# Performance work log

Hardware: AMD Instinct MI355X
Metric: run time of the kernel (lower is better)

## Reference

```python
import jax, jax.numpy as jnp
import numpy as np

N_HEAD = 12
NUM_BLOCK_TOKENS = 64
SSMAX_S_INIT = 0.43


def setup_inputs() -> dict:
    key = jax.random.key(0)
    k1, k2, k3 = jax.random.split(key, 3)
    B, T, C = 2, 2048, 768
    x = jax.random.normal(k1, (B, T, C), dtype=jnp.float32)
    # torch Linear weights: y = x @ W.T ; init scaled for stability
    c_attn_w = jax.random.normal(k2, (3 * C, C), dtype=jnp.float32) * 0.02
    c_proj_w = jax.random.normal(k3, (C, C), dtype=jnp.float32) * 0.02
    s = jnp.full((1,), SSMAX_S_INIT, dtype=jnp.float32)  # learnable SSMax scale
    return {"x": x, "c_attn_w": c_attn_w, "c_proj_w": c_proj_w, "s": s}


def reference(x, c_attn_w, c_proj_w, s):
    B, T, C = x.shape
    H, hd, n = N_HEAD, C // N_HEAD, NUM_BLOCK_TOKENS
    qkv = x @ c_attn_w.T                              # [B,T,3C]
    q, k, v = jnp.split(qkv, 3, axis=-1)
    q = q.reshape(B, T, H, hd).transpose(0, 2, 1, 3)  # [B,H,T,hd]
    k = k.reshape(B, T, H, hd).transpose(0, 2, 1, 3)
    v = v.reshape(B, T, H, hd).transpose(0, 2, 1, 3)
    att = jnp.einsum('bhqd,bhkd->bhqk', q, k) * (1.0 / np.sqrt(hd))
    # slot-based block mask reduces to block-causal: allow s_idx//n <= t_idx//n
    blk = jnp.arange(T) // n
    mask = blk[:, None] >= blk[None, :]               # [T,T] bool, True=attend
    scale = s[0] * np.log(T).astype(np.float32)       # SSMax: s * log(N)
    att = jnp.where(mask[None, None], att * scale, -jnp.inf)
    att = jax.nn.softmax(att, axis=-1)
    y = jnp.einsum('bhqk,bhkd->bhqd', att, v)
    y = y.transpose(0, 2, 1, 3).reshape(B, T, C)
    return y @ c_proj_w.T
```

## Files before the change

### kernel.cpp

```cpp
#include <hip/hip_runtime.h>
#include <hip/hip_bf16.h>
#include <stdint.h>

#define T_SEQ 2048
#define C_DIM 768
#define NH 12
#define HD 64
#define QK_LD 1536

typedef __attribute__((ext_vector_type(8))) short short8;
typedef __attribute__((ext_vector_type(4))) float f32x4;
typedef const __attribute__((address_space(1))) void* gas_ptr;
typedef __attribute__((address_space(3))) void* las_ptr;

static __device__ __forceinline__ unsigned short f2bf(float f) {
  union { float f; unsigned u; } c; c.f = f;
  unsigned u = c.u + 0x7fffu + ((c.u >> 16) & 1u);
  return (unsigned short)(u >> 16);
}

__global__ void cast3_kernel(const float* __restrict__ a, int na4,
                             const float* __restrict__ b, int nb4,
                             const float* __restrict__ c, int nc4,
                             unsigned short* __restrict__ oa,
                             unsigned short* __restrict__ ob,
                             unsigned short* __restrict__ oc) {
  int i = blockIdx.x * blockDim.x + threadIdx.x;
  int stride = gridDim.x * blockDim.x;
  int total = na4 + nb4 + nc4;
  for (; i < total; i += stride) {
    const float4* src; ushort4* dst; int j;
    if (i < na4)            { src = (const float4*)a; dst = (ushort4*)oa; j = i; }
    else if (i < na4 + nb4) { src = (const float4*)b; dst = (ushort4*)ob; j = i - na4; }
    else                    { src = (const float4*)c; dst = (ushort4*)oc; j = i - na4 - nb4; }
    float4 v = src[j];
    ushort4 o;
    o.x = f2bf(v.x); o.y = f2bf(v.y); o.z = f2bf(v.z); o.w = f2bf(v.w);
    dst[j] = o;
  }
}

__global__ void zero2_kernel(float4* __restrict__ a, int n4a,
                             float4* __restrict__ b, int n4b) {
  int i = blockIdx.x * blockDim.x + threadIdx.x;
  int stride = gridDim.x * blockDim.x;
  float4 z = {0.f, 0.f, 0.f, 0.f};
  for (int j = i; j < n4a; j += stride) a[j] = z;
  for (int j = i; j < n4b; j += stride) b[j] = z;
}

template <int NP>
__device__ __forceinline__ void stage_tile(const unsigned short* g, int ld,
                                           unsigned short* ldsbase, int tid) {
#pragma unroll
  for (int p = 0; p < NP; ++p) {
    int j = p * 256 + tid;
    int row = j >> 2, cc = (j & 3) << 3;
    const unsigned short* ga = g + (size_t)row * ld + cc;
    unsigned short* la = ldsbase + p * 2048 + (tid >> 6) * 512;
    __builtin_amdgcn_global_load_lds((gas_ptr)ga, (las_ptr)la, 16, 0, 0);
  }
}

template <int BM, int EPI>
__launch_bounds__(256, 2)
__global__ void gemm_bt(const unsigned short* __restrict__ A,
                        const unsigned short* __restrict__ B,
                        int K,
                        unsigned short* __restrict__ obf,
                        unsigned short* __restrict__ vt,
                        float* __restrict__ ofp,
                        const float* __restrict__ sptr) {
  constexpr int MI = BM / 32;
  constexpr int LDS_SH = BM * 32 + 4096;
  constexpr int TR_SH = (EPI == 0) ? 128 * 130 : 0;
  constexpr int TOT = LDS_SH > TR_SH ? LDS_SH : TR_SH;
  __shared__ __attribute__((aligned(16))) unsigned short smem[TOT];
  unsigned short* lds = smem;
  int tid = threadIdx.x;
  int lane = tid & 63, wave = tid >> 6;
  int row0 = blockIdx.x * BM, col0 = blockIdx.y * 128;
  int wr = (wave >> 1) * (BM / 2), wc = (wave & 1) * 64;
  int la = lane & 15, lb = lane >> 4;
  f32x4 acc[MI][4] = {};

  for (int k0 = 0; k0 < K; k0 += 32) {
    __syncthreads();
    stage_tile<BM / 64>(A + (size_t)row0 * K + k0, K, lds, tid);
    stage_tile<2>(B + (size_t)col0 * K + k0, K, lds + BM * 32, tid);
    __syncthreads();
    short8 af[MI], bfr[4];
#pragma unroll
    for (int i = 0; i < MI; ++i)
      af[i] = *(const short8*)&lds[(wr + i * 16 + la) * 32 + lb * 8];
#pragma unroll
    for (int j = 0; j < 4; ++j)
      bfr[j] = *(const short8*)&lds[BM * 32 + (wc + j * 16 + la) * 32 + lb * 8];
#pragma unroll
    for (int i = 0; i < MI; ++i)
#pragma unroll
      for (int j = 0; j < 4; ++j)
        acc[i][j] = __builtin_amdgcn_mfma_f32_16x16x32_bf16(af[i], bfr[j], acc[i][j], 0, 0, 0);
  }

  if (EPI == 0 && col0 >= 1536) {
    __syncthreads();
#pragma unroll
    for (int i = 0; i < MI; ++i)
#pragma unroll
      for (int j = 0; j < 4; ++j)
#pragma unroll
        for (int r = 0; r < 4; ++r)
          smem[(wr + i * 16 + lb * 4 + r) * 130 + (wc + j * 16 + la)] =
              f2bf(acc[i][j][r]);
    __syncthreads();
    int bb = row0 >> 11, t0 = row0 & 2047;
    int cl = tid >> 1, half = tid & 1;
    int vcol = col0 - 1536 + cl;
    int h = vcol >> 6, d = vcol & 63;
    unsigned short* dst =
        vt + ((size_t)(bb * NH + h) * 64 + d) * T_SEQ + t0 + half * 64;
#pragma unroll
    for (int j = 0; j < 8; ++j) {
      short8 v8;
#pragma unroll
      for (int e = 0; e < 8; ++e)
        v8[e] = (short)smem[(half * 64 + j * 8 + e) * 130 + cl];
      *(short8*)(dst + j * 8) = v8;
    }
    return;
  }

  float qs = 0.f;
  if (EPI == 0)
    qs = sptr[0] * 7.624618986159398f  * 0.125f
         * 1.4426950408889634f ;
#pragma unroll
  for (int i = 0; i < MI; ++i) {
    int gr0 = row0 + wr + i * 16 + lb * 4;
#pragma unroll
    for (int j = 0; j < 4; ++j) {
      int gc = col0 + wc + j * 16 + la;
#pragma unroll
      for (int r = 0; r < 4; ++r) {
        float v = acc[i][j][r];
        int rr = gr0 + r;
        if (EPI == 0) {
          obf[(size_t)rr * QK_LD + gc] = f2bf(gc < 768 ? v * qs : v);
        } else {
          ofp[(size_t)rr * C_DIM + gc] = v;
        }
      }
    }
  }
}

__device__ __forceinline__ void attn_stage(const unsigned short* kg,
                                           const unsigned short* vg,
                                           char* kbuf, int wave, int lane) {
  int l3 = lane >> 3;
  int cg = ((lane & 7) ^ l3) << 4;
#pragma unroll
  for (int q = 0; q < 2; ++q) {
    int rk = q * 32 + wave * 8 + l3;
    const unsigned short* ka = kg + (size_t)rk * QK_LD + (cg >> 1);
    char* kl = kbuf + (q * 32 + wave * 8) * 128;
    __builtin_amdgcn_global_load_lds((gas_ptr)ka, (las_ptr)kl, 16, 0, 0);
    const unsigned short* va = vg + (size_t)rk * T_SEQ + (cg >> 1);
    char* vl = kbuf + 8192 + (q * 32 + wave * 8) * 128;
    __builtin_amdgcn_global_load_lds((gas_ptr)va, (las_ptr)vl, 16, 0, 0);
  }
}

__launch_bounds__(256, 4)
__global__ void attn_kernel(const unsigned short* __restrict__ qkb,
                            const unsigned short* __restrict__ vt,
                            float* __restrict__ yp,
                            float* __restrict__ lsp) {
  __shared__ __attribute__((aligned(16))) char smem[2 * 16384 + 8192];

  int tid = threadIdx.x, lane = tid & 63, wave = tid >> 6;
  int la = lane & 15, lb = lane >> 4;
  int xx = 47 - (int)blockIdx.x;
  int qi, cch;
  if (xx < 16) { qi = xx; cch = 0; }
  else         { int t = xx - 16; qi = 16 + (t >> 1); cch = t & 1; }
  int kt0 = cch * 16;
  int kt1 = min(qi, kt0 + 15);
  int bh = blockIdx.y;
  int b = bh / NH, h = bh - b * NH;

  const unsigned short* qbase =
      qkb + ((size_t)(b * T_SEQ + qi * 64 + wave * 16 + la)) * QK_LD + h * HD;
  short8 qf0 = *(const short8*)(qbase + lb * 8);
  short8 qf1 = *(const short8*)(qbase + 32 + lb * 8);
  asm volatile("" :: "v"(qf0), "v"(qf1));

  f32x4 y[4] = {};
  float ls[4] = {0.f, 0.f, 0.f, 0.f};

  const unsigned short* kg0 = qkb + (size_t)b * T_SEQ * QK_LD + 768 + h * HD;
  const unsigned short* vg0 = vt + (size_t)bh * 64 * T_SEQ;
  char* pw = smem + 32768 + wave * 2048;

  attn_stage(kg0 + (size_t)kt0 * 64 * QK_LD, vg0 + kt0 * 64, smem, wave, lane);
  int cur = 0;

  for (int kt = kt0; kt <= kt1; ++kt) {
    asm volatile("" ::: "memory");
    __builtin_amdgcn_s_barrier();
    if (kt < kt1) {
      attn_stage(kg0 + (size_t)(kt + 1) * 64 * QK_LD, vg0 + (kt + 1) * 64,
                 smem + ((cur ^ 1) * 16384), wave, lane);
      asm volatile("s_waitcnt vmcnt(4)" ::: "memory");
    } else {
      asm volatile("s_waitcnt vmcnt(0)" ::: "memory");
    }
    __builtin_amdgcn_s_barrier();
    asm volatile("" ::: "memory");
    __builtin_amdgcn_sched_barrier(0);

    char* kl = smem + cur * 16384;
    char* vl = kl + 8192;

    f32x4 s[4] = {};
    __builtin_amdgcn_s_setprio(1);
#pragma unroll
    for (int fk = 0; fk < 4; ++fk) {
      int row = fk * 16 + la;
      {
        int off = (row * 128 + 0 * 64 + lb * 16) ^ ((row & 7) << 4);
        short8 kf = *(const short8*)(kl + off);
        s[fk] = __builtin_amdgcn_mfma_f32_16x16x32_bf16(qf0, kf, s[fk], 0, 0, 0);
      }
      {
        int off = (row * 128 + 1 * 64 + lb * 16) ^ ((row & 7) << 4);
        short8 kf = *(const short8*)(kl + off);
        s[fk] = __builtin_amdgcn_mfma_f32_16x16x32_bf16(qf1, kf, s[fk], 0, 0, 0);
      }
    }
    __builtin_amdgcn_s_setprio(0);

#pragma unroll
    for (int fk = 0; fk < 4; ++fk)
#pragma unroll
      for (int r = 0; r < 4; ++r) {
        float p = __builtin_amdgcn_exp2f(s[fk][r]);
        s[fk][r] = p;
        ls[r] += p;
        int row = lb * 4 + r;
        int off = (row * 128 + (fk * 16 + la) * 2) ^ ((row & 7) << 4);
        *(unsigned short*)(pw + off) = f2bf(p);
      }

    short8 pa[2];
#pragma unroll
    for (int ch = 0; ch < 2; ++ch) {
      int off = (la * 128 + ch * 64 + lb * 16) ^ ((la & 7) << 4);
      pa[ch] = *(const short8*)(pw + off);
    }
    __builtin_amdgcn_s_setprio(1);
#pragma unroll
    for (int fd = 0; fd < 4; ++fd) {
      int row = fd * 16 + la;
#pragma unroll
      for (int ch = 0; ch < 2; ++ch) {
        int off = (row * 128 + ch * 64 + lb * 16) ^ ((row & 7) << 4);
        short8 vf = *(const short8*)(vl + off);
        y[fd] = __builtin_amdgcn_mfma_f32_16x16x32_bf16(pa[ch], vf, y[fd], 0, 0, 0);
      }
    }
    __builtin_amdgcn_s_setprio(0);

    cur ^= 1;
  }

  size_t slotbase = (size_t)cch * (24 * 2048);
#pragma unroll
  for (int r = 0; r < 4; ++r) {
    float v = ls[r];
    v += __shfl_xor(v, 1); v += __shfl_xor(v, 2);
    v += __shfl_xor(v, 4); v += __shfl_xor(v, 8);
    ls[r] = v;
  }
  int trow = qi * 64 + wave * 16 + lb * 4;
  if (la == 0) {
#pragma unroll
    for (int r = 0; r < 4; ++r)
      lsp[slotbase + (size_t)bh * 2048 + trow + r] = ls[r];
  }
  float* ydst = yp + (slotbase + (size_t)bh * 2048) * 64;
#pragma unroll
  for (int fd = 0; fd < 4; ++fd)
#pragma unroll
    for (int r = 0; r < 4; ++r)
      ydst[(size_t)(trow + r) * 64 + fd * 16 + la] = y[fd][r];
}

__global__ void norm_kernel(const float* __restrict__ yp,
                            const float* __restrict__ lsp,
                            unsigned short* __restrict__ yb) {
  int gid = blockIdx.x * blockDim.x + threadIdx.x;
  int dq = gid & 15;
  int row = gid >> 4;
  int bh = row >> 11, t = row & 2047;
  int b = bh / NH, h = bh - b * NH;
  float denom = lsp[row] + lsp[24 * 2048 + row];
  float inv = 1.0f / denom;
  float4 y0 = ((const float4*)yp)[row * 16 + dq];
  float4 y1 = ((const float4*)yp)[(24 * 2048 * 16) + row * 16 + dq];
  ushort4 o;
  o.x = f2bf((y0.x + y1.x) * inv);
  o.y = f2bf((y0.y + y1.y) * inv);
  o.z = f2bf((y0.z + y1.z) * inv);
  o.w = f2bf((y0.w + y1.w) * inv);
  ((ushort4*)yb)[(size_t)(b * T_SEQ + t) * 192 + h * 16 + dq] = o;
}

extern "C" void kernel_launch(void* const* d_in, const int* in_sizes, int n_in,
                              void* d_out, int out_size, void* d_ws, size_t ws_size,
                              hipStream_t stream) {
  const float* x = (const float*)d_in[0];
  const float* attn_w = (const float*)d_in[1];
  const float* proj_w = (const float*)d_in[2];
  const float* s = (const float*)d_in[3];
  float* out = (float*)d_out;

  char* ws = (char*)d_ws;
  unsigned short* xb  = (unsigned short*)(ws);
  unsigned short* wab = (unsigned short*)(ws + 6291456);
  unsigned short* wpb = (unsigned short*)(ws + 9830400);
  unsigned short* qkb = (unsigned short*)(ws + 11010048);
  unsigned short* vtb = (unsigned short*)(ws + 23592960);
  unsigned short* yb  = (unsigned short*)(ws + 29884416);
  float*          yp  = (float*)(ws + 36175872);
  float*          lsp = (float*)(ws + 61341696);

  cast3_kernel<<<2048, 256, 0, stream>>>(x, 3145728 / 4, attn_w, 1769472 / 4,
                                         proj_w, 589824 / 4, xb, wab, wpb);

  zero2_kernel<<<1024, 256, 0, stream>>>((float4*)(yp + 24 * 2048 * 64), 786432,
                                         (float4*)(lsp + 24 * 2048), 12288);

  gemm_bt<128, 0><<<dim3(32, 18), 256, 0, stream>>>(xb, wab, 768, qkb, vtb, nullptr, s);

  attn_kernel<<<dim3(48, 24), 256, 0, stream>>>(qkb, vtb, yp, lsp);

  norm_kernel<<<3072, 256, 0, stream>>>(yp, lsp, yb);

  gemm_bt<64, 1><<<dim3(64, 6), 256, 0, stream>>>(yb, wpb, 768, nullptr, nullptr, out, nullptr);
}
```

Measured before the change: 163.7 us.

## Double-buffer GEMM LDS, remap blocks per XCD, normalize single-chunk attention rows in-kernel

The GEMM K loop now double-buffers LDS tiles, prefetching the next K slice while MFMAs run on the current one, and occupancy hints are raised. Block indices in both the GEMMs and the attention kernel are remapped so neighbouring tiles land on the same XCD, aiming at better L2 reuse. Attention blocks for the first 16 query tiles, which have only one key chunk, normalize and write bf16 output directly. This removes the zero kernel and halves the norm kernel's work. The changes cost extra LDS per block and more complex index arithmetic.

```diff
diff --git a/kernel.cpp b/kernel.cpp
--- a/kernel.cpp
+++ b/kernel.cpp
@@ -40,15 +40,6 @@
   }
 }
 
-__global__ void zero2_kernel(float4* __restrict__ a, int n4a,
-                             float4* __restrict__ b, int n4b) {
-  int i = blockIdx.x * blockDim.x + threadIdx.x;
-  int stride = gridDim.x * blockDim.x;
-  float4 z = {0.f, 0.f, 0.f, 0.f};
-  for (int j = i; j < n4a; j += stride) a[j] = z;
-  for (int j = i; j < n4b; j += stride) b[j] = z;
-}
-
 template <int NP>
 __device__ __forceinline__ void stage_tile(const unsigned short* g, int ld,
                                            unsigned short* ldsbase, int tid) {
@@ -62,8 +53,8 @@
   }
 }
 
-template <int BM, int EPI>
-__launch_bounds__(256, 2)
+template <int BM, int EPI, int NY, int PERX>
+__launch_bounds__(256, EPI == 0 ? 3 : 4)
 __global__ void gemm_bt(const unsigned short* __restrict__ A,
                         const unsigned short* __restrict__ B,
                         int K,
@@ -72,39 +63,51 @@
                         float* __restrict__ ofp,
                         const float* __restrict__ sptr) {
   constexpr int MI = BM / 32;
-  constexpr int LDS_SH = BM * 32 + 4096;
+  constexpr int ABUF = BM * 32;
+  constexpr int BUF = ABUF + 4096;
+  constexpr int LDS_SH = 2 * BUF;
   constexpr int TR_SH = (EPI == 0) ? 128 * 130 : 0;
   constexpr int TOT = LDS_SH > TR_SH ? LDS_SH : TR_SH;
   __shared__ __attribute__((aligned(16))) unsigned short smem[TOT];
-  unsigned short* lds = smem;
   int tid = threadIdx.x;
   int lane = tid & 63, wave = tid >> 6;
-  int row0 = blockIdx.x * BM, col0 = blockIdx.y * 128;
+  int L = blockIdx.x;
+  int t0 = (L & 7) * PERX + (L >> 3);
+  int row0 = (t0 / NY) * BM, col0 = (t0 % NY) * 128;
   int wr = (wave >> 1) * (BM / 2), wc = (wave & 1) * 64;
   int la = lane & 15, lb = lane >> 4;
   f32x4 acc[MI][4] = {};
 
-  for (int k0 = 0; k0 < K; k0 += 32) {
-    __syncthreads();
-    stage_tile<BM / 64>(A + (size_t)row0 * K + k0, K, lds, tid);
-    stage_tile<2>(B + (size_t)col0 * K + k0, K, lds + BM * 32, tid);
-    __syncthreads();
+  const unsigned short* Abase = A + (size_t)row0 * K;
+  const unsigned short* Bbase = B + (size_t)col0 * K;
+  stage_tile<BM / 64>(Abase, K, smem, tid);
+  stage_tile<2>(Bbase, K, smem + ABUF, tid);
+  __syncthreads();
+  int cur = 0;
+  int nt = K >> 5;
+  for (int t = 0; t < nt; ++t) {
+    if (t + 1 < nt) {
+      stage_tile<BM / 64>(Abase + (t + 1) * 32, K, smem + (cur ^ 1) * BUF, tid);
+      stage_tile<2>(Bbase + (t + 1) * 32, K, smem + (cur ^ 1) * BUF + ABUF, tid);
+    }
+    unsigned short* lds = smem + cur * BUF;
     short8 af[MI], bfr[4];
 #pragma unroll
     for (int i = 0; i < MI; ++i)
       af[i] = *(const short8*)&lds[(wr + i * 16 + la) * 32 + lb * 8];
 #pragma unroll
     for (int j = 0; j < 4; ++j)
-      bfr[j] = *(const short8*)&lds[BM * 32 + (wc + j * 16 + la) * 32 + lb * 8];
+      bfr[j] = *(const short8*)&lds[ABUF + (wc + j * 16 + la) * 32 + lb * 8];
 #pragma unroll
     for (int i = 0; i < MI; ++i)
 #pragma unroll
       for (int j = 0; j < 4; ++j)
         acc[i][j] = __builtin_amdgcn_mfma_f32_16x16x32_bf16(af[i], bfr[j], acc[i][j], 0, 0, 0);
+    __syncthreads();
+    cur ^= 1;
   }
 
   if (EPI == 0 && col0 >= 1536) {
-    __syncthreads();
 #pragma unroll
     for (int i = 0; i < MI; ++i)
 #pragma unroll
@@ -114,12 +117,12 @@
           smem[(wr + i * 16 + lb * 4 + r) * 130 + (wc + j * 16 + la)] =
               f2bf(acc[i][j][r]);
     __syncthreads();
-    int bb = row0 >> 11, t0 = row0 & 2047;
+    int bb = row0 >> 11, t0r = row0 & 2047;
     int cl = tid >> 1, half = tid & 1;
     int vcol = col0 - 1536 + cl;
     int h = vcol >> 6, d = vcol & 63;
     unsigned short* dst =
-        vt + ((size_t)(bb * NH + h) * 64 + d) * T_SEQ + t0 + half * 64;
+        vt + ((size_t)(bb * NH + h) * 64 + d) * T_SEQ + t0r + half * 64;
 #pragma unroll
     for (int j = 0; j < 8; ++j) {
       short8 v8;
@@ -176,18 +179,21 @@
 __global__ void attn_kernel(const unsigned short* __restrict__ qkb,
                             const unsigned short* __restrict__ vt,
                             float* __restrict__ yp,
-                            float* __restrict__ lsp) {
+                            float* __restrict__ lsp,
+                            unsigned short* __restrict__ yb) {
   __shared__ __attribute__((aligned(16))) char smem[2 * 16384 + 8192];
 
   int tid = threadIdx.x, lane = tid & 63, wave = tid >> 6;
   int la = lane & 15, lb = lane >> 4;
-  int xx = 47 - (int)blockIdx.x;
+  int L = blockIdx.x;
+  int ixcd = L >> 3;
+  int bh = (L & 7) * 3 + ixcd / 48;
+  int xx = 47 - (ixcd % 48);
   int qi, cch;
   if (xx < 16) { qi = xx; cch = 0; }
   else         { int t = xx - 16; qi = 16 + (t >> 1); cch = t & 1; }
   int kt0 = cch * 16;
   int kt1 = min(qi, kt0 + 15);
-  int bh = blockIdx.y;
   int b = bh / NH, h = bh - b * NH;
 
   const unsigned short* qbase =
@@ -275,7 +281,6 @@
     cur ^= 1;
   }
 
-  size_t slotbase = (size_t)cch * (24 * 2048);
 #pragma unroll
   for (int r = 0; r < 4; ++r) {
     float v = ls[r];
@@ -284,17 +289,33 @@
     ls[r] = v;
   }
   int trow = qi * 64 + wave * 16 + lb * 4;
-  if (la == 0) {
-#pragma unroll
-    for (int r = 0; r < 4; ++r)
-      lsp[slotbase + (size_t)bh * 2048 + trow + r] = ls[r];
-  }
-  float* ydst = yp + (slotbase + (size_t)bh * 2048) * 64;
-#pragma unroll
-  for (int fd = 0; fd < 4; ++fd)
-#pragma unroll
-    for (int r = 0; r < 4; ++r)
-      ydst[(size_t)(trow + r) * 64 + fd * 16 + la] = y[fd][r];
+
+  if (qi < 16) {
+    float inv[4];
+#pragma unroll
+    for (int r = 0; r < 4; ++r) inv[r] = 1.0f / ls[r];
+#pragma unroll
+    for (int fd = 0; fd < 4; ++fd)
+#pragma unroll
+      for (int r = 0; r < 4; ++r) {
+        int rowg = b * T_SEQ + trow + r;
+        int colg = h * HD + fd * 16 + la;
+        yb[(size_t)rowg * C_DIM + colg] = f2bf(y[fd][r] * inv[r]);
+      }
+  } else {
+    size_t slotbase = (size_t)cch * (24 * 2048);
+    if (la == 0) {
+#pragma unroll
+      for (int r = 0; r < 4; ++r)
+        lsp[slotbase + (size_t)bh * 2048 + trow + r] = ls[r];
+    }
+    float* ydst = yp + (slotbase + (size_t)bh * 2048) * 64;
+#pragma unroll
+    for (int fd = 0; fd < 4; ++fd)
+#pragma unroll
+      for (int r = 0; r < 4; ++r)
+        ydst[(size_t)(trow + r) * 64 + fd * 16 + la] = y[fd][r];
+  }
 }
 
 __global__ void norm_kernel(const float* __restrict__ yp,
@@ -302,8 +323,9 @@
                             unsigned short* __restrict__ yb) {
   int gid = blockIdx.x * blockDim.x + threadIdx.x;
   int dq = gid & 15;
-  int row = gid >> 4;
-  int bh = row >> 11, t = row & 2047;
+  int rloc = gid >> 4;
+  int bh = rloc >> 10, t = 1024 + (rloc & 1023);
+  int row = bh * 2048 + t;
   int b = bh / NH, h = bh - b * NH;
   float denom = lsp[row] + lsp[24 * 2048 + row];
   float inv = 1.0f / denom;
@@ -339,14 +361,11 @@
   cast3_kernel<<<2048, 256, 0, stream>>>(x, 3145728 / 4, attn_w, 1769472 / 4,
                                          proj_w, 589824 / 4, xb, wab, wpb);
 
-  zero2_kernel<<<1024, 256, 0, stream>>>((float4*)(yp + 24 * 2048 * 64), 786432,
-                                         (float4*)(lsp + 24 * 2048), 12288);
-
-  gemm_bt<128, 0><<<dim3(32, 18), 256, 0, stream>>>(xb, wab, 768, qkb, vtb, nullptr, s);
-
-  attn_kernel<<<dim3(48, 24), 256, 0, stream>>>(qkb, vtb, yp, lsp);
-
-  norm_kernel<<<3072, 256, 0, stream>>>(yp, lsp, yb);
-
-  gemm_bt<64, 1><<<dim3(64, 6), 256, 0, stream>>>(yb, wpb, 768, nullptr, nullptr, out, nullptr);
-}
+  gemm_bt<128, 0, 18, 72><<<576, 256, 0, stream>>>(xb, wab, 768, qkb, vtb, nullptr, s);
+
+  attn_kernel<<<1152, 256, 0, stream>>>(qkb, vtb, yp, lsp, yb);
+
+  norm_kernel<<<1536, 256, 0, stream>>>(yp, lsp, yb);
+
+  gemm_bt<64, 1, 6, 48><<<384, 256, 0, stream>>>(yb, wpb, 768, nullptr, nullptr, out, nullptr);
+}
```

Result: faster. 149.3 us (-8.8%).
